# Kernel tuning notes

Hardware: AMD Instinct MI355X
Metric: run time of the kernel (lower is better)

## Reference

```python
import jax, jax.numpy as jnp
import numpy as np
import math

B, N, E, H = 16, 1024, 512, 8
DH = E // H

def setup_inputs() -> dict:
    key = jax.random.key(0)
    ks = jax.random.split(key, 12)
    inp = {
        "q": jax.random.normal(ks[0], (B, N, E), dtype=jnp.float32),
        "k": jax.random.normal(ks[1], (B, N, E), dtype=jnp.float32),
        "v": jax.random.normal(ks[2], (B, N, E), dtype=jnp.float32),
        "d": jax.random.uniform(ks[3], (B, N, N), dtype=jnp.float32),
        # nn.Linear weights (out, in) with orthogonal-ish init scaled small, zero bias
        "Wq": jax.random.normal(ks[4], (E, E), dtype=jnp.float32) * 0.01,
        "bq": jnp.zeros((E,), dtype=jnp.float32),
        "Wk": jax.random.normal(ks[5], (E, E), dtype=jnp.float32) * 0.01,
        "bk": jnp.zeros((E,), dtype=jnp.float32),
        "Wv": jax.random.normal(ks[6], (E, E), dtype=jnp.float32) * 0.01,
        "bv": jnp.zeros((E,), dtype=jnp.float32),
        "Wp": jax.random.normal(ks[7], (E, E), dtype=jnp.float32) * 0.01,
        "bp": jnp.zeros((E,), dtype=jnp.float32),
    }
    return inp

def _heads(x, W, b):
    # torch Linear: x @ W.T + b, then split heads -> [B, H, N, DH]
    y = jnp.einsum('bne,fe->bnf', x, W) + b
    return y.reshape(x.shape[0], x.shape[1], H, DH).transpose(0, 2, 1, 3)

def reference(q, k, v, d, Wq, bq, Wk, bk, Wv, bv, Wp, bp):
    qh = _heads(q, Wq, bq)                                  # [B,H,N,DH]
    kh = _heads(k, Wk, bk)
    vh = _heads(v, Wv, bv)
    scale = 1.0 / math.sqrt(DH)
    att = jnp.einsum('bhnd,bhmd->bhnm', qh, kh) * scale     # [B,H,N,N]
    db = d[:, None, :, :]                                   # broadcast over heads
    att = jax.nn.softmax(att + db, axis=-1)
    att = att * db                                          # multiplicative distance bias post-softmax
    x = jnp.einsum('bhnm,bhmd->bhnd', att, vh)              # [B,H,N,DH]
    x = x.transpose(0, 2, 1, 3).reshape(q.shape[0], q.shape[1], E)
    return jnp.einsum('bne,fe->bnf', x, Wp) + bp
```

## Files before the change

kernel.cpp:

```cpp
#include <hip/hip_runtime.h>
#include <hip/hip_bf16.h>


#define Bc  16
#define Nc  1024
#define Ec  512
#define Hc  8
#define DHc 64

typedef float  f32x4  __attribute__((ext_vector_type(4)));
typedef short  s16x4  __attribute__((ext_vector_type(4)));
typedef short  s16x8  __attribute__((ext_vector_type(8)));
typedef __bf16 bf16x8 __attribute__((ext_vector_type(8)));

static __device__ __forceinline__ f32x4 mfma16(s16x8 a, s16x8 b, f32x4 c) {
    return __builtin_amdgcn_mfma_f32_16x16x32_bf16(
        __builtin_bit_cast(bf16x8, a), __builtin_bit_cast(bf16x8, b), c, 0, 0, 0);
}

static __device__ __forceinline__ unsigned short f2bf(float f) {
    return __builtin_bit_cast(unsigned short, __float2bfloat16(f));
}

static __device__ __forceinline__ s16x8 pack_bf16(f32x4 a, f32x4 b) {
    s16x8 r;
    r[0] = (short)f2bf(a[0]); r[1] = (short)f2bf(a[1]);
    r[2] = (short)f2bf(a[2]); r[3] = (short)f2bf(a[3]);
    r[4] = (short)f2bf(b[0]); r[5] = (short)f2bf(b[1]);
    r[6] = (short)f2bf(b[2]); r[7] = (short)f2bf(b[3]);
    return r;
}

static __device__ __forceinline__ void gld16(const void* g, void* l) {
    __builtin_amdgcn_global_load_lds(
        (const __attribute__((address_space(1))) void*)g,
        (__attribute__((address_space(3))) void*)l, 16, 0, 0);
}

__global__ __launch_bounds__(256) void wcvt_kernel(
    const float* __restrict__ Wq, const float* __restrict__ Wk,
    const float* __restrict__ Wv, const float* __restrict__ Wp,
    unsigned short* __restrict__ wbf)
{
    const int seg = blockIdx.x >> 7;
    const float* src = seg == 0 ? Wq : (seg == 1 ? Wk : (seg == 2 ? Wv : Wp));
    const int g = (blockIdx.x & 127) * 256 + threadIdx.x;
    const float* p = src + (size_t)g * 8;
    f32x4 a = *(const f32x4*)p, b = *(const f32x4*)(p + 4);
    *(s16x8*)(wbf + (size_t)seg * 262144 + (size_t)g * 8) = pack_bf16(a, b);
}

__global__ __launch_bounds__(256) void proj3_kernel(
    const float* __restrict__ qi, const float* __restrict__ ki,
    const float* __restrict__ vi, const unsigned short* __restrict__ wbf,
    const float* __restrict__ bq, const float* __restrict__ bk,
    const float* __restrict__ bv,
    unsigned short* __restrict__ qo, unsigned short* __restrict__ ko,
    unsigned short* __restrict__ vo)
{
    const int z = blockIdx.z;
    const float* Af = z == 0 ? qi : (z == 1 ? ki : vi);
    const unsigned short* Wb = wbf + (size_t)z * 262144;
    const float* bias = z == 0 ? bq : (z == 1 ? bk : bv);
    unsigned short* out = z == 0 ? qo : (z == 1 ? ko : vo);
    const int mode = (z == 2) ? 1 : 0;

    __shared__ float As_raw[128 * 32];
    __shared__ unsigned short Bsb[128 * 32];

    const int tid = threadIdx.x;
    const int w = tid >> 6, lane = tid & 63;
    const int lr = lane & 15, grp = lane >> 4;
    const int wr = w >> 1, wc = w & 1;
    const int m0 = blockIdx.x * 128, n0 = blockIdx.y * 128;

    f32x4 acc[4][4];
#pragma unroll
    for (int i = 0; i < 4; ++i)
#pragma unroll
        for (int j = 0; j < 4; ++j) acc[i][j] = (f32x4)(0.0f);

    const int h8 = lane >> 3, l8 = lane & 7;
    const int fcol = ((l8 ^ h8) << 2);
    const int h4 = lane >> 2, l4 = lane & 3;
    const int bcol = ((l4 ^ (h4 & 3)) << 3);
    const int o0 = (((grp << 1) ^ (lr & 7)) << 2);
    const int ob = ((grp ^ (lr & 3)) << 3);

    for (int k0 = 0; k0 < Ec; k0 += 32) {
        __syncthreads();
#pragma unroll
        for (int i = 0; i < 4; ++i) {
            const int chunk = i * 4 + w;
            const int row = chunk * 8 + h8;
            gld16(Af + (size_t)(m0 + row) * Ec + k0 + fcol,
                  (char*)As_raw + chunk * 1024 + lane * 16);
        }
#pragma unroll
        for (int i = 0; i < 2; ++i) {
            const int chunk = i * 4 + w;
            const int row = chunk * 16 + h4;
            gld16(Wb + (size_t)(n0 + row) * Ec + k0 + bcol,
                  (char*)Bsb + chunk * 1024 + lane * 16);
        }
        __syncthreads();

        s16x8 afr[4], bfr[4];
#pragma unroll
        for (int mi = 0; mi < 4; ++mi) {
            const float* p = As_raw + (wr * 64 + mi * 16 + lr) * 32;
            afr[mi] = pack_bf16(*(const f32x4*)(p + o0), *(const f32x4*)(p + (o0 ^ 4)));
        }
#pragma unroll
        for (int ni = 0; ni < 4; ++ni)
            bfr[ni] = *(const s16x8*)(Bsb + (wc * 64 + ni * 16 + lr) * 32 + ob);
#pragma unroll
        for (int mi = 0; mi < 4; ++mi)
#pragma unroll
            for (int ni = 0; ni < 4; ++ni)
                acc[mi][ni] = mfma16(afr[mi], bfr[ni], acc[mi][ni]);
    }

#pragma unroll
    for (int mi = 0; mi < 4; ++mi) {
        const int mbase = m0 + wr * 64 + mi * 16 + grp * 4;
#pragma unroll
        for (int ni = 0; ni < 4; ++ni) {
            const int f = n0 + wc * 64 + ni * 16 + lr;
            const float bi = bias[f];
            f32x4 vv = acc[mi][ni];
            const int hh = f >> 6, dh = f & 63;
            if (mode == 0) {
#pragma unroll
                for (int r = 0; r < 4; ++r) {
                    const int m = mbase + r;
                    out[(((size_t)(m >> 10) * Hc + hh) * Nc + (m & (Nc - 1))) * DHc + dh] =
                        f2bf(vv[r] + bi);
                }
            } else {
                const int bb = mbase >> 10, n = mbase & (Nc - 1);
                s16x4 pk;
#pragma unroll
                for (int r = 0; r < 4; ++r) pk[r] = (short)f2bf(vv[r] + bi);
                *(s16x4*)&out[(((size_t)bb * Hc + hh) * DHc + dh) * Nc + n] = pk;
            }
        }
    }
}

__global__ __launch_bounds__(256) void outproj_kernel(
    const unsigned short* __restrict__ Ab, const unsigned short* __restrict__ Wb,
    const float* __restrict__ bias, float* __restrict__ out)
{
    __shared__ unsigned short Asb[128 * 32];
    __shared__ unsigned short Bsb[128 * 32];

    const int tid = threadIdx.x;
    const int w = tid >> 6, lane = tid & 63;
    const int lr = lane & 15, grp = lane >> 4;
    const int wr = w >> 1, wc = w & 1;
    const int m0 = blockIdx.x * 128, n0 = blockIdx.y * 128;

    f32x4 acc[4][4];
#pragma unroll
    for (int i = 0; i < 4; ++i)
#pragma unroll
        for (int j = 0; j < 4; ++j) acc[i][j] = (f32x4)(0.0f);

    const int h4 = lane >> 2, l4 = lane & 3;
    const int bcol = ((l4 ^ (h4 & 3)) << 3);
    const int ob = ((grp ^ (lr & 3)) << 3);

    for (int k0 = 0; k0 < Ec; k0 += 32) {
        __syncthreads();
#pragma unroll
        for (int i = 0; i < 2; ++i) {
            const int chunk = i * 4 + w;
            const int row = chunk * 16 + h4;
            gld16(Ab + (size_t)(m0 + row) * Ec + k0 + bcol,
                  (char*)Asb + chunk * 1024 + lane * 16);
            gld16(Wb + (size_t)(n0 + row) * Ec + k0 + bcol,
                  (char*)Bsb + chunk * 1024 + lane * 16);
        }
        __syncthreads();

        s16x8 afr[4], bfr[4];
#pragma unroll
        for (int mi = 0; mi < 4; ++mi)
            afr[mi] = *(const s16x8*)(Asb + (wr * 64 + mi * 16 + lr) * 32 + ob);
#pragma unroll
        for (int ni = 0; ni < 4; ++ni)
            bfr[ni] = *(const s16x8*)(Bsb + (wc * 64 + ni * 16 + lr) * 32 + ob);
#pragma unroll
        for (int mi = 0; mi < 4; ++mi)
#pragma unroll
            for (int ni = 0; ni < 4; ++ni)
                acc[mi][ni] = mfma16(afr[mi], bfr[ni], acc[mi][ni]);
    }

#pragma unroll
    for (int mi = 0; mi < 4; ++mi) {
        const int mbase = m0 + wr * 64 + mi * 16 + grp * 4;
#pragma unroll
        for (int ni = 0; ni < 4; ++ni) {
            const int f = n0 + wc * 64 + ni * 16 + lr;
            const float bi = bias[f];
            f32x4 vv = acc[mi][ni];
#pragma unroll
            for (int r = 0; r < 4; ++r)
                out[(size_t)(mbase + r) * Ec + f] = vv[r] + bi;
        }
    }
}

__global__ __launch_bounds__(256) void attn_kernel(
    const unsigned short* __restrict__ qh, const unsigned short* __restrict__ kh,
    const unsigned short* __restrict__ vt, const float* __restrict__ dmat,
    unsigned short* __restrict__ xh)
{
    __shared__ unsigned short K_lds[64 * 64];
    __shared__ unsigned short V_lds[64 * 64];
    __shared__ unsigned short P_lds[4][32][72];

    const int lin = blockIdx.x;
    const int swz = ((lin & 7) << 7) | (lin >> 3);
    const int qt = swz & 7, h = (swz >> 3) & 7, b = swz >> 6;

    const int tid = threadIdx.x;
    const int w = tid >> 6, lane = tid & 63;
    const int lr = lane & 15, grp = lane >> 4;
    const int h8 = lane >> 3, l8 = lane & 7;
    const int q0 = qt * 128;
    const int bh = b * Hc + h;
    const int qw = q0 + w * 32;
    const int kofs = grp * 4;
    const int scol = (l8 ^ h8) * 8;
    const float* dbase0 = dmat + ((size_t)b * Nc + qw + lr) * Nc;
    const float* dbase1 = dbase0 + (size_t)16 * Nc;

    const float LOG2E = 1.4426950408889634f;
    const float SC    = 0.125f * LOG2E;
    const float MC    = -4.0f * LOG2E;

    s16x8 bq0[2], bq1[2];
#pragma unroll
    for (int ks = 0; ks < 2; ++ks) {
        bq0[ks] = *reinterpret_cast<const s16x8*>(
            qh + ((size_t)bh * Nc + qw + lr) * DHc + ks * 32 + grp * 8);
        bq1[ks] = *reinterpret_cast<const s16x8*>(
            qh + ((size_t)bh * Nc + qw + 16 + lr) * DHc + ks * 32 + grp * 8);
    }

    f32x4 acc0[4], acc1[4];
#pragma unroll
    for (int c = 0; c < 4; ++c) { acc0[c] = (f32x4)(0.0f); acc1[c] = (f32x4)(0.0f); }
    float lsum0 = 0.f, lsum1 = 0.f;

    for (int kt = 0; kt < Nc / 64; ++kt) {
        const int k0 = kt * 64;
        __syncthreads();
#pragma unroll
        for (int i = 0; i < 2; ++i) {
            const int ch = w + i * 4;
            gld16(kh + ((size_t)bh * Nc + k0 + ch * 8 + h8) * DHc + scol,
                  (char*)K_lds + ch * 1024 + lane * 16);
            gld16(vt + ((size_t)bh * DHc + ch * 8 + h8) * Nc + k0 + scol,
                  (char*)V_lds + ch * 1024 + lane * 16);
        }
        f32x4 dv0[4], dv1[4];
#pragma unroll
        for (int c = 0; c < 4; ++c) {
            dv0[c] = *reinterpret_cast<const f32x4*>(dbase0 + k0 + c * 16 + kofs);
            dv1[c] = *reinterpret_cast<const f32x4*>(dbase1 + k0 + c * 16 + kofs);
        }
        __syncthreads();

        f32x4 lgt0[4], lgt1[4];
#pragma unroll
        for (int c = 0; c < 4; ++c) { lgt0[c] = (f32x4)(0.0f); lgt1[c] = (f32x4)(0.0f); }
        __builtin_amdgcn_s_setprio(1);
#pragma unroll
        for (int ks = 0; ks < 2; ++ks) {
#pragma unroll
            for (int c = 0; c < 4; ++c) {
                const int row = c * 16 + lr;
                const int slot = (4 * ks + grp) ^ (lr & 7);
                s16x8 ak = *reinterpret_cast<const s16x8*>(
                    (const char*)K_lds + row * 128 + slot * 16);
                lgt0[c] = mfma16(ak, bq0[ks], lgt0[c]);
                lgt1[c] = mfma16(ak, bq1[ks], lgt1[c]);
            }
        }
        __builtin_amdgcn_s_setprio(0);
#pragma unroll
        for (int c = 0; c < 4; ++c) {
            s16x4 pk0, pk1;
#pragma unroll
            for (int r = 0; r < 4; ++r) {
                const float dl0 = fmaf(dv0[c][r], LOG2E, MC);
                const float p0 = __builtin_amdgcn_exp2f(fmaf(lgt0[c][r], SC, dl0));
                lsum0 += p0;
                pk0[r] = (short)f2bf(p0 * dv0[c][r]);
                const float dl1 = fmaf(dv1[c][r], LOG2E, MC);
                const float p1 = __builtin_amdgcn_exp2f(fmaf(lgt1[c][r], SC, dl1));
                lsum1 += p1;
                pk1[r] = (short)f2bf(p1 * dv1[c][r]);
            }
            *reinterpret_cast<s16x4*>(&P_lds[w][lr][c * 16 + kofs]) = pk0;
            *reinterpret_cast<s16x4*>(&P_lds[w][16 + lr][c * 16 + kofs]) = pk1;
        }
        __builtin_amdgcn_s_setprio(1);
#pragma unroll
        for (int ks = 0; ks < 2; ++ks) {
            s16x8 pa0 = *reinterpret_cast<const s16x8*>(&P_lds[w][lr][ks * 32 + grp * 8]);
            s16x8 pa1 = *reinterpret_cast<const s16x8*>(&P_lds[w][16 + lr][ks * 32 + grp * 8]);
#pragma unroll
            for (int c = 0; c < 4; ++c) {
                const int row = c * 16 + lr;
                const int slot = (4 * ks + grp) ^ (lr & 7);
                s16x8 bv = *reinterpret_cast<const s16x8*>(
                    (const char*)V_lds + row * 128 + slot * 16);
                acc0[c] = mfma16(pa0, bv, acc0[c]);
                acc1[c] = mfma16(pa1, bv, acc1[c]);
            }
        }
        __builtin_amdgcn_s_setprio(0);
    }
    lsum0 += __shfl_xor(lsum0, 16, 64);
    lsum0 += __shfl_xor(lsum0, 32, 64);
    lsum1 += __shfl_xor(lsum1, 16, 64);
    lsum1 += __shfl_xor(lsum1, 32, 64);
    const float invd0 = 1.0f / lsum0, invd1 = 1.0f / lsum1;
    float inv0[4], inv1[4];
#pragma unroll
    for (int r = 0; r < 4; ++r) {
        inv0[r] = __shfl(invd0, grp * 4 + r, 64);
        inv1[r] = __shfl(invd1, grp * 4 + r, 64);
    }
#pragma unroll
    for (int c = 0; c < 4; ++c)
#pragma unroll
        for (int r = 0; r < 4; ++r) {
            xh[((size_t)b * Nc + qw + grp * 4 + r) * Ec + h * DHc + c * 16 + lr] =
                f2bf(acc0[c][r] * inv0[r]);
            xh[((size_t)b * Nc + qw + 16 + grp * 4 + r) * Ec + h * DHc + c * 16 + lr] =
                f2bf(acc1[c][r] * inv1[r]);
        }
}

extern "C" void kernel_launch(void* const* d_in, const int* in_sizes, int n_in,
                              void* d_out, int out_size, void* d_ws, size_t ws_size,
                              hipStream_t stream)
{
    (void)in_sizes; (void)n_in; (void)out_size; (void)ws_size;
    const float* q  = (const float*)d_in[0];
    const float* k  = (const float*)d_in[1];
    const float* v  = (const float*)d_in[2];
    const float* dm = (const float*)d_in[3];
    const float* Wq = (const float*)d_in[4];
    const float* bq = (const float*)d_in[5];
    const float* Wk = (const float*)d_in[6];
    const float* bk = (const float*)d_in[7];
    const float* Wv = (const float*)d_in[8];
    const float* bv = (const float*)d_in[9];
    const float* Wp = (const float*)d_in[10];
    const float* bp = (const float*)d_in[11];
    float* out = (float*)d_out;

    const size_t sz = (size_t)Bc * Hc * Nc * DHc;
    unsigned short* qhb = (unsigned short*)d_ws;
    unsigned short* khb = qhb + sz;
    unsigned short* vtb = khb + sz;
    unsigned short* xhb = vtb + sz;
    unsigned short* wbf = xhb + sz;

    wcvt_kernel<<<dim3(512), dim3(256), 0, stream>>>(Wq, Wk, Wv, Wp, wbf);
    proj3_kernel<<<dim3(Bc * Nc / 128, Ec / 128, 3), dim3(256), 0, stream>>>(
        q, k, v, wbf, bq, bk, bv, qhb, khb, vtb);
    attn_kernel<<<dim3(Bc * Hc * Nc / 128), dim3(256), 0, stream>>>(
        qhb, khb, vtb, dm, xhb);
    outproj_kernel<<<dim3(Bc * Nc / 128, Ec / 128), dim3(256), 0, stream>>>(
        xhb, wbf + (size_t)3 * 262144, bp, out);
}
```

Before: 167.6 us.

## Register-prefetch next K/V and distance tiles to overlap loads with compute

Replaces direct global-to-LDS loads with register staging: the next tile's K, V and distance values are issued as global loads into registers while the current tile is computed, then written to LDS at the top of the next iteration. The two __syncthreads per iteration become a waitcnt-plus-barrier after the LDS stores and a plain barrier after the PV MFMAs. The goal is to hide global memory latency behind the MFMA and softmax work. It costs extra VGPRs for the staged tiles, which may lower occupancy.

```diff
diff --git a/kernel.cpp b/kernel.cpp
--- a/kernel.cpp
+++ b/kernel.cpp
@@ -9,6 +9,7 @@
 #define DHc 64
 
 typedef float  f32x4  __attribute__((ext_vector_type(4)));
+typedef int    i32x4  __attribute__((ext_vector_type(4)));
 typedef short  s16x4  __attribute__((ext_vector_type(4)));
 typedef short  s16x8  __attribute__((ext_vector_type(8)));
 typedef __bf16 bf16x8 __attribute__((ext_vector_type(8)));
@@ -35,6 +36,17 @@
     __builtin_amdgcn_global_load_lds(
         (const __attribute__((address_space(1))) void*)g,
         (__attribute__((address_space(3))) void*)l, 16, 0, 0);
+}
+
+static __device__ __forceinline__ void lds_publish_barrier() {
+    asm volatile("s_waitcnt lgkmcnt(0)" ::: "memory");
+    __builtin_amdgcn_s_barrier();
+    asm volatile("" ::: "memory");
+}
+static __device__ __forceinline__ void plain_barrier() {
+    asm volatile("" ::: "memory");
+    __builtin_amdgcn_s_barrier();
+    asm volatile("" ::: "memory");
 }
 
 __global__ __launch_bounds__(256) void wcvt_kernel(
@@ -256,24 +268,42 @@
     for (int c = 0; c < 4; ++c) { acc0[c] = (f32x4)(0.0f); acc1[c] = (f32x4)(0.0f); }
     float lsum0 = 0.f, lsum1 = 0.f;
 
-    for (int kt = 0; kt < Nc / 64; ++kt) {
-        const int k0 = kt * 64;
-        __syncthreads();
+    const int NT = Nc / 64;
+    i32x4 kst[2], vst[2];
+#pragma unroll
+    for (int i = 0; i < 2; ++i) {
+        const int ch = w + i * 4;
+        kst[i] = *reinterpret_cast<const i32x4*>(
+            kh + ((size_t)bh * Nc + ch * 8 + h8) * DHc + scol);
+        vst[i] = *reinterpret_cast<const i32x4*>(
+            vt + ((size_t)bh * DHc + ch * 8 + h8) * Nc + scol);
+    }
+    f32x4 dv0[4], dv1[4];
+#pragma unroll
+    for (int c = 0; c < 4; ++c) {
+        dv0[c] = *reinterpret_cast<const f32x4*>(dbase0 + c * 16 + kofs);
+        dv1[c] = *reinterpret_cast<const f32x4*>(dbase1 + c * 16 + kofs);
+    }
+
+    for (int kt = 0; kt < NT; ++kt) {
 #pragma unroll
         for (int i = 0; i < 2; ++i) {
             const int ch = w + i * 4;
-            gld16(kh + ((size_t)bh * Nc + k0 + ch * 8 + h8) * DHc + scol,
-                  (char*)K_lds + ch * 1024 + lane * 16);
-            gld16(vt + ((size_t)bh * DHc + ch * 8 + h8) * Nc + k0 + scol,
-                  (char*)V_lds + ch * 1024 + lane * 16);
-        }
-        f32x4 dv0[4], dv1[4];
-#pragma unroll
-        for (int c = 0; c < 4; ++c) {
-            dv0[c] = *reinterpret_cast<const f32x4*>(dbase0 + k0 + c * 16 + kofs);
-            dv1[c] = *reinterpret_cast<const f32x4*>(dbase1 + k0 + c * 16 + kofs);
-        }
-        __syncthreads();
+            *reinterpret_cast<i32x4*>((char*)K_lds + ch * 1024 + lane * 16) = kst[i];
+            *reinterpret_cast<i32x4*>((char*)V_lds + ch * 1024 + lane * 16) = vst[i];
+        }
+        if (kt + 1 < NT) {
+            const int k1 = (kt + 1) * 64;
+#pragma unroll
+            for (int i = 0; i < 2; ++i) {
+                const int ch = w + i * 4;
+                kst[i] = *reinterpret_cast<const i32x4*>(
+                    kh + ((size_t)bh * Nc + k1 + ch * 8 + h8) * DHc + scol);
+                vst[i] = *reinterpret_cast<const i32x4*>(
+                    vt + ((size_t)bh * DHc + ch * 8 + h8) * Nc + k1 + scol);
+            }
+        }
+        lds_publish_barrier();
 
         f32x4 lgt0[4], lgt1[4];
 #pragma unroll
@@ -309,6 +339,14 @@
             *reinterpret_cast<s16x4*>(&P_lds[w][lr][c * 16 + kofs]) = pk0;
             *reinterpret_cast<s16x4*>(&P_lds[w][16 + lr][c * 16 + kofs]) = pk1;
         }
+        if (kt + 1 < NT) {
+            const int k1 = (kt + 1) * 64;
+#pragma unroll
+            for (int c = 0; c < 4; ++c) {
+                dv0[c] = *reinterpret_cast<const f32x4*>(dbase0 + k1 + c * 16 + kofs);
+                dv1[c] = *reinterpret_cast<const f32x4*>(dbase1 + k1 + c * 16 + kofs);
+            }
+        }
         __builtin_amdgcn_s_setprio(1);
 #pragma unroll
         for (int ks = 0; ks < 2; ++ks) {
@@ -325,6 +363,7 @@
             }
         }
         __builtin_amdgcn_s_setprio(0);
+        plain_barrier();
     }
     lsum0 += __shfl_xor(lsum0, 16, 64);
     lsum0 += __shfl_xor(lsum0, 32, 64);
```

After: 158.5 us. 1.06x faster.

## Share distance-matrix tile across all heads in one block, read K/V directly

Applied to the files above, without the earlier changes.

Restructures the attention kernel so each 512-thread block handles 32 query rows for all 8 heads, one wave per head. The fp32 distance tile is then loaded once into double-buffered LDS and shared across heads instead of being re-read from global memory per head. K and V fragments are now read straight from global memory (cached) instead of being staged in LDS. This cuts the dominant d-matrix traffic by the head count, at the cost of uncoalesced K/V global loads with no LDS reuse and fewer, larger blocks.

```diff
diff --git a/kernel.cpp b/kernel.cpp
--- a/kernel.cpp
+++ b/kernel.cpp
@@ -35,6 +35,12 @@
     __builtin_amdgcn_global_load_lds(
         (const __attribute__((address_space(1))) void*)g,
         (__attribute__((address_space(3))) void*)l, 16, 0, 0);
+}
+
+static __device__ __forceinline__ void lds_publish_barrier() {
+    asm volatile("s_waitcnt lgkmcnt(0)" ::: "memory");
+    __builtin_amdgcn_s_barrier();
+    asm volatile("" ::: "memory");
 }
 
 __global__ __launch_bounds__(256) void wcvt_kernel(
@@ -213,30 +219,31 @@
     }
 }
 
-__global__ __launch_bounds__(256) void attn_kernel(
+__global__ __launch_bounds__(512) void attn_kernel(
     const unsigned short* __restrict__ qh, const unsigned short* __restrict__ kh,
     const unsigned short* __restrict__ vt, const float* __restrict__ dmat,
     unsigned short* __restrict__ xh)
 {
-    __shared__ unsigned short K_lds[64 * 64];
-    __shared__ unsigned short V_lds[64 * 64];
-    __shared__ unsigned short P_lds[4][32][72];
+    __shared__ float D_lds[2][32 * 64];
+    __shared__ unsigned short P_lds[8][32][72];
 
     const int lin = blockIdx.x;
-    const int swz = ((lin & 7) << 7) | (lin >> 3);
-    const int qt = swz & 7, h = (swz >> 3) & 7, b = swz >> 6;
+    const int j = lin >> 3;
+    const int b = ((lin & 7) << 1) | (j >> 5);
+    const int qt = j & 31;
+    const int q0 = qt * 32;
 
     const int tid = threadIdx.x;
     const int w = tid >> 6, lane = tid & 63;
     const int lr = lane & 15, grp = lane >> 4;
-    const int h8 = lane >> 3, l8 = lane & 7;
-    const int q0 = qt * 128;
-    const int bh = b * Hc + h;
-    const int qw = q0 + w * 32;
+    const int bh = b * Hc + w;
     const int kofs = grp * 4;
-    const int scol = (l8 ^ h8) * 8;
-    const float* dbase0 = dmat + ((size_t)b * Nc + qw + lr) * Nc;
-    const float* dbase1 = dbase0 + (size_t)16 * Nc;
+
+    const int drow = w * 4 + (lane >> 4);
+    const int dslot = lane & 15;
+    const int dcol = ((dslot ^ (drow & 15)) << 2);
+    const float* dsrc = dmat + ((size_t)b * Nc + q0 + drow) * Nc + dcol;
+    const int dldsoff = w * 1024 + lane * 16;
 
     const float LOG2E = 1.4426950408889634f;
     const float SC    = 0.125f * LOG2E;
@@ -246,9 +253,9 @@
 #pragma unroll
     for (int ks = 0; ks < 2; ++ks) {
         bq0[ks] = *reinterpret_cast<const s16x8*>(
-            qh + ((size_t)bh * Nc + qw + lr) * DHc + ks * 32 + grp * 8);
+            qh + ((size_t)bh * Nc + q0 + lr) * DHc + ks * 32 + grp * 8);
         bq1[ks] = *reinterpret_cast<const s16x8*>(
-            qh + ((size_t)bh * Nc + qw + 16 + lr) * DHc + ks * 32 + grp * 8);
+            qh + ((size_t)bh * Nc + q0 + 16 + lr) * DHc + ks * 32 + grp * 8);
     }
 
     f32x4 acc0[4], acc1[4];
@@ -256,24 +263,29 @@
     for (int c = 0; c < 4; ++c) { acc0[c] = (f32x4)(0.0f); acc1[c] = (f32x4)(0.0f); }
     float lsum0 = 0.f, lsum1 = 0.f;
 
-    for (int kt = 0; kt < Nc / 64; ++kt) {
+    f32x4 dst = *reinterpret_cast<const f32x4*>(dsrc);
+    *reinterpret_cast<f32x4*>((char*)D_lds[0] + dldsoff) = dst;
+    dst = *reinterpret_cast<const f32x4*>(dsrc + 64);
+
+    const int NT = Nc / 64;
+    for (int kt = 0; kt < NT; ++kt) {
+        const int cur = kt & 1;
         const int k0 = kt * 64;
-        __syncthreads();
-#pragma unroll
-        for (int i = 0; i < 2; ++i) {
-            const int ch = w + i * 4;
-            gld16(kh + ((size_t)bh * Nc + k0 + ch * 8 + h8) * DHc + scol,
-                  (char*)K_lds + ch * 1024 + lane * 16);
-            gld16(vt + ((size_t)bh * DHc + ch * 8 + h8) * Nc + k0 + scol,
-                  (char*)V_lds + ch * 1024 + lane * 16);
-        }
+        lds_publish_barrier();
+        if (kt + 1 < NT)
+            *reinterpret_cast<f32x4*>((char*)D_lds[cur ^ 1] + dldsoff) = dst;
+        if (kt + 2 < NT)
+            dst = *reinterpret_cast<const f32x4*>(dsrc + (kt + 2) * 64);
+
         f32x4 dv0[4], dv1[4];
 #pragma unroll
         for (int c = 0; c < 4; ++c) {
-            dv0[c] = *reinterpret_cast<const f32x4*>(dbase0 + k0 + c * 16 + kofs);
-            dv1[c] = *reinterpret_cast<const f32x4*>(dbase1 + k0 + c * 16 + kofs);
-        }
-        __syncthreads();
+            const int sl = ((c * 4 + grp) ^ lr) * 16;
+            dv0[c] = *reinterpret_cast<const f32x4*>(
+                (const char*)D_lds[cur] + lr * 256 + sl);
+            dv1[c] = *reinterpret_cast<const f32x4*>(
+                (const char*)D_lds[cur] + (16 + lr) * 256 + sl);
+        }
 
         f32x4 lgt0[4], lgt1[4];
 #pragma unroll
@@ -283,10 +295,8 @@
         for (int ks = 0; ks < 2; ++ks) {
 #pragma unroll
             for (int c = 0; c < 4; ++c) {
-                const int row = c * 16 + lr;
-                const int slot = (4 * ks + grp) ^ (lr & 7);
                 s16x8 ak = *reinterpret_cast<const s16x8*>(
-                    (const char*)K_lds + row * 128 + slot * 16);
+                    kh + ((size_t)bh * Nc + k0 + c * 16 + lr) * DHc + ks * 32 + grp * 8);
                 lgt0[c] = mfma16(ak, bq0[ks], lgt0[c]);
                 lgt1[c] = mfma16(ak, bq1[ks], lgt1[c]);
             }
@@ -316,10 +326,8 @@
             s16x8 pa1 = *reinterpret_cast<const s16x8*>(&P_lds[w][16 + lr][ks * 32 + grp * 8]);
 #pragma unroll
             for (int c = 0; c < 4; ++c) {
-                const int row = c * 16 + lr;
-                const int slot = (4 * ks + grp) ^ (lr & 7);
                 s16x8 bv = *reinterpret_cast<const s16x8*>(
-                    (const char*)V_lds + row * 128 + slot * 16);
+                    vt + ((size_t)bh * DHc + c * 16 + lr) * Nc + k0 + ks * 32 + grp * 8);
                 acc0[c] = mfma16(pa0, bv, acc0[c]);
                 acc1[c] = mfma16(pa1, bv, acc1[c]);
             }
@@ -341,9 +349,9 @@
     for (int c = 0; c < 4; ++c)
 #pragma unroll
         for (int r = 0; r < 4; ++r) {
-            xh[((size_t)b * Nc + qw + grp * 4 + r) * Ec + h * DHc + c * 16 + lr] =
+            xh[((size_t)b * Nc + q0 + grp * 4 + r) * Ec + w * DHc + c * 16 + lr] =
                 f2bf(acc0[c][r] * inv0[r]);
-            xh[((size_t)b * Nc + qw + 16 + grp * 4 + r) * Ec + h * DHc + c * 16 + lr] =
+            xh[((size_t)b * Nc + q0 + 16 + grp * 4 + r) * Ec + w * DHc + c * 16 + lr] =
                 f2bf(acc1[c][r] * inv1[r]);
         }
 }
@@ -377,7 +385,7 @@
     wcvt_kernel<<<dim3(512), dim3(256), 0, stream>>>(Wq, Wk, Wv, Wp, wbf);
     proj3_kernel<<<dim3(Bc * Nc / 128, Ec / 128, 3), dim3(256), 0, stream>>>(
         q, k, v, wbf, bq, bk, bv, qhb, khb, vtb);
-    attn_kernel<<<dim3(Bc * Hc * Nc / 128), dim3(256), 0, stream>>>(
+    attn_kernel<<<dim3(Bc * Nc / 32), dim3(512), 0, stream>>>(
         qhb, khb, vtb, dm, xhb);
     outproj_kernel<<<dim3(Bc * Nc / 128, Ec / 128), dim3(256), 0, stream>>>(
         xhb, wbf + (size_t)3 * 262144, bp, out);
```

After: 215.9 us. +28.8%, slower.
